# Kernel tuning notes

Hardware: AMD Instinct MI355X
Metric: run time of the kernel (lower is better)

The kernel has to match this reference:

```python
import jax, jax.numpy as jnp
import numpy as np

B, S, D, H = 4, 2048, 512, 8
HD = D // H  # head_dim = 64


def setup_inputs() -> dict:
    key = jax.random.key(0)
    ks = jax.random.split(key, 10)
    scale = 1.0 / np.sqrt(D)  # keep activations O(1)
    x = jax.random.normal(ks[0], (B, S, D), dtype=jnp.float32)
    # causal mask, broadcast over batch and heads
    causal = jnp.tril(jnp.ones((S, S), dtype=bool))
    mask = jnp.broadcast_to(causal, (B, H, S, S))
    def lin(k):
        return jax.random.normal(k, (D, D), dtype=jnp.float32) * scale
    return {
        "x": x,
        "mask": mask,
        "Wq": lin(ks[1]), "bq": jax.random.normal(ks[2], (D,), dtype=jnp.float32) * 0.01,
        "Wk": lin(ks[3]), "bk": jax.random.normal(ks[4], (D,), dtype=jnp.float32) * 0.01,
        "Wv": lin(ks[5]), "bv": jax.random.normal(ks[6], (D,), dtype=jnp.float32) * 0.01,
        "Wo": lin(ks[7]), "bo": jax.random.normal(ks[8], (D,), dtype=jnp.float32) * 0.01,
    }


def reference(x, mask, Wq, bq, Wk, bk, Wv, bv, Wo, bo):
    # eqx.nn.Linear computes W @ x + b per row; batched form is x @ W.T + b.
    b, s, d = x.shape
    q = jnp.einsum("bsd,ed->bse", x, Wq) + bq
    k = jnp.einsum("bsd,ed->bse", x, Wk) + bk
    v = jnp.einsum("bsd,ed->bse", x, Wv) + bv
    # [B, H, S, HD]
    q = q.reshape(b, s, H, HD).transpose(0, 2, 1, 3)
    k = k.reshape(b, s, H, HD).transpose(0, 2, 1, 3)
    v = v.reshape(b, s, H, HD).transpose(0, 2, 1, 3)
    scores = jnp.einsum("bhqd,bhkd->bhqk", q, k) / jnp.sqrt(jnp.asarray(HD, x.dtype))
    scores = jnp.where(mask, scores, jnp.asarray(-1e9, x.dtype))
    attn = jax.nn.softmax(scores, axis=-1)
    attended = jnp.einsum("bhqk,bhkd->bhqd", attn, v)
    attended = attended.transpose(0, 2, 1, 3).reshape(b, s, d)
    out = jnp.einsum("bsd,ed->bse", attended, Wo) + bo
    return out
```

## Files before the change

### kernel.cpp

```cpp
#include <hip/hip_runtime.h>

#define S_LEN 2048
#define DM    512
#define NH    8
#define HD    64

typedef unsigned short u16;
typedef unsigned int   u32;
typedef __bf16 bf16_t;
typedef bf16_t bf16x8 __attribute__((ext_vector_type(8)));
typedef float  f32x4  __attribute__((ext_vector_type(4)));

__device__ __forceinline__ u16 f2bf(float f) {
    u32 u = __float_as_uint(f);
    u += 0x7FFFu + ((u >> 16) & 1u);
    return (u16)(u >> 16);
}

__device__ __forceinline__ void g2l16(const u16* g, u16* l) {
    __builtin_amdgcn_global_load_lds(
        (const __attribute__((address_space(1))) u32*)g,
        (__attribute__((address_space(3))) u32*)l,
        16, 0, 0);
}

__device__ __forceinline__ float qmax16(float v) {
    v = fmaxf(v, __shfl_xor(v, 1));
    v = fmaxf(v, __shfl_xor(v, 2));
    v = fmaxf(v, __shfl_xor(v, 4));
    v = fmaxf(v, __shfl_xor(v, 8));
    return v;
}
__device__ __forceinline__ float qsum16(float v) {
    v += __shfl_xor(v, 1);
    v += __shfl_xor(v, 2);
    v += __shfl_xor(v, 4);
    v += __shfl_xor(v, 8);
    return v;
}

__global__ __launch_bounds__(256) void cvt_bf16(
    const float* __restrict__ x,
    const float* __restrict__ wq, const float* __restrict__ wk,
    const float* __restrict__ wv, const float* __restrict__ wo,
    u16* __restrict__ xb, u16* __restrict__ wqb, u16* __restrict__ wkb,
    u16* __restrict__ wvb, u16* __restrict__ wob)
{
    const int y = blockIdx.y;
    const float* src; u16* dst; int n;
    if (y == 0)      { src = x;  dst = xb;  n = 4 * S_LEN * DM; }
    else if (y == 1) { src = wq; dst = wqb; n = DM * DM; }
    else if (y == 2) { src = wk; dst = wkb; n = DM * DM; }
    else if (y == 3) { src = wv; dst = wvb; n = DM * DM; }
    else             { src = wo; dst = wob; n = DM * DM; }
    int idx = (blockIdx.x * 256 + threadIdx.x) * 8;
    if (idx >= n) return;
    float4 f0 = *(const float4*)(src + idx);
    float4 f1 = *(const float4*)(src + idx + 4);
    u32 p0 = (u32)f2bf(f0.x) | ((u32)f2bf(f0.y) << 16);
    u32 p1 = (u32)f2bf(f0.z) | ((u32)f2bf(f0.w) << 16);
    u32 p2 = (u32)f2bf(f1.x) | ((u32)f2bf(f1.y) << 16);
    u32 p3 = (u32)f2bf(f1.z) | ((u32)f2bf(f1.w) << 16);
    *(uint4*)(dst + idx) = make_uint4(p0, p1, p2, p3);
}

__global__ __launch_bounds__(256) void qkv_gemm(
    const u16* __restrict__ xb,
    const u16* __restrict__ Wqb, const u16* __restrict__ Wkb, const u16* __restrict__ Wvb,
    const float* __restrict__ bq, const float* __restrict__ bk, const float* __restrict__ bv,
    u16* __restrict__ Qb, u16* __restrict__ Kb, u16* __restrict__ Vb)
{
    __shared__ u16 Als[4096];
    __shared__ u16 Bls[4096];

    const int t = threadIdx.x;
    const int lane = t & 63, w = t >> 6;
    const int ln = lane & 15, quad = lane >> 4;
    const int wm = w >> 1, wn = w & 1;
    const int m0 = blockIdx.x * 128;
    const int mat = blockIdx.y >> 2;
    const int n0 = (blockIdx.y & 3) * 128;

    const u16* __restrict__ Wb     = (mat == 0) ? Wqb : (mat == 1) ? Wkb : Wvb;
    const float* __restrict__ bias = (mat == 0) ? bq : (mat == 1) ? bk : bv;
    u16* __restrict__ outp         = (mat == 0) ? Qb : (mat == 1) ? Kb : Vb;

    const int ch0 = (w * 2 + 0) * 64 + lane;
    const int ch1 = (w * 2 + 1) * 64 + lane;
    const int sr0 = ch0 >> 2, sk0 = (ch0 & 3) ^ ((sr0 >> 1) & 3);
    const int sr1 = ch1 >> 2, sk1 = (ch1 & 3) ^ ((sr1 >> 1) & 3);
    const u16* pA0 = xb + (size_t)(m0 + sr0) * DM + sk0 * 8;
    const u16* pA1 = xb + (size_t)(m0 + sr1) * DM + sk1 * 8;
    const u16* pB0 = Wb + (size_t)(n0 + sr0) * DM + sk0 * 8;
    const u16* pB1 = Wb + (size_t)(n0 + sr1) * DM + sk1 * 8;
    u16* lds0 = (u16*)((w * 2 + 0) * 512);
    u16* lds1 = (u16*)((w * 2 + 1) * 512);
    u16* lA0 = Als + (w * 2 + 0) * 512;
    u16* lA1 = Als + (w * 2 + 1) * 512;
    u16* lB0 = Bls + (w * 2 + 0) * 512;
    u16* lB1 = Bls + (w * 2 + 1) * 512;
    (void)lds0; (void)lds1;

    f32x4 acc[4][4] = {};
    for (int k0 = 0; k0 < DM; k0 += 32) {
        __syncthreads();
        g2l16(pA0 + k0, lA0);
        g2l16(pA1 + k0, lA1);
        g2l16(pB0 + k0, lB0);
        g2l16(pB1 + k0, lB1);
        __syncthreads();
        bf16x8 af[4], bf8[4];
        #pragma unroll
        for (int i = 0; i < 4; ++i) {
            int row = wm * 64 + i * 16 + ln;
            af[i] = *(const bf16x8*)(Als + (row * 4 + (quad ^ ((row >> 1) & 3))) * 8);
        }
        #pragma unroll
        for (int j = 0; j < 4; ++j) {
            int row = wn * 64 + j * 16 + ln;
            bf8[j] = *(const bf16x8*)(Bls + (row * 4 + (quad ^ ((row >> 1) & 3))) * 8);
        }
        #pragma unroll
        for (int i = 0; i < 4; ++i)
            #pragma unroll
            for (int j = 0; j < 4; ++j)
                acc[i][j] = __builtin_amdgcn_mfma_f32_16x16x32_bf16(af[i], bf8[j], acc[i][j], 0, 0, 0);
    }

    #pragma unroll
    for (int j = 0; j < 4; ++j) {
        int colg = n0 + wn * 64 + j * 16 + ln;
        float bj = bias[colg];
        int h = colg >> 6, d = colg & 63;
        #pragma unroll
        for (int i = 0; i < 4; ++i) {
            int mbase = m0 + wm * 64 + i * 16 + quad * 4;
            #pragma unroll
            for (int r = 0; r < 4; ++r) {
                int m = mbase + r;
                int bb = m >> 11, s = m & 2047;
                outp[(((size_t)bb * NH + h) * S_LEN + s) * HD + d] = f2bf(acc[i][j][r] + bj);
            }
        }
    }
}

__global__ __launch_bounds__(256) void attn_mfma(
    const u16* __restrict__ Qb, const u16* __restrict__ Kb, const u16* __restrict__ Vb,
    u16* __restrict__ Attb)
{
    __shared__ u16 Qls[4096];
    __shared__ u16 Kls[4096];
    __shared__ u16 Vt[4096];
    __shared__ u16 Ps[4096];

    const int t = threadIdx.x;
    const int lane = t & 63, w = t >> 6;
    const int ln = lane & 15, quad = lane >> 4;
    const int bh = blockIdx.y;
    const int qt = (blockIdx.x + bh) & 31;
    const int q_base = qt * 64;
    const size_t base = (size_t)bh * S_LEN * HD;

    {
        const int c0 = (w * 2 + 0) * 64 + lane;
        const int c1 = (w * 2 + 1) * 64 + lane;
        const int r0 = c0 >> 3, k0 = (c0 & 7) ^ (r0 & 7);
        const int r1 = c1 >> 3, k1 = (c1 & 7) ^ (r1 & 7);
        g2l16(Qb + base + (size_t)(q_base + r0) * HD + k0 * 8, Qls + (w * 2 + 0) * 512);
        g2l16(Qb + base + (size_t)(q_base + r1) * HD + k1 * 8, Qls + (w * 2 + 1) * 512);
    }
    __syncthreads();

    bf16x8 aq[2];
    #pragma unroll
    for (int ks = 0; ks < 2; ++ks) {
        int row = w * 16 + ln;
        aq[ks] = *(const bf16x8*)(Qls + (row * 8 + ((ks * 4 + quad) ^ (row & 7))) * 8);
    }

    const int ck0 = (w * 2 + 0) * 64 + lane;
    const int ck1 = (w * 2 + 1) * 64 + lane;
    const int kr0 = ck0 >> 3, kk0 = (ck0 & 7) ^ (kr0 & 7);
    const int kr1 = ck1 >> 3, kk1 = (ck1 & 7) ^ (kr1 & 7);
    const u16* pK0 = Kb + base + (size_t)kr0 * HD + kk0 * 8;
    const u16* pK1 = Kb + base + (size_t)kr1 * HD + kk1 * 8;
    u16* lK0 = Kls + (w * 2 + 0) * 512;
    u16* lK1 = Kls + (w * 2 + 1) * 512;

    const int vkey0 = t >> 3,        vd0 = (t & 7) * 8;
    const int vkey1 = (t + 256) >> 3;
    const u16* pV0 = Vb + base + (size_t)vkey0 * HD + vd0;
    const u16* pV1 = Vb + base + (size_t)vkey1 * HD + vd0;

    float m_st[4], l_st[4], alpha[4];
    f32x4 o[4] = {};
    #pragma unroll
    for (int r = 0; r < 4; ++r) { m_st[r] = -1e30f; l_st[r] = 0.f; }

    const float sc = 0.125f * 1.44269504f;
    const int qrow_base = q_base + w * 16;

    for (int kt = 0; kt <= qt; ++kt) {
        __syncthreads();
        g2l16(pK0 + (size_t)kt * 64 * HD, lK0);
        g2l16(pK1 + (size_t)kt * 64 * HD, lK1);
        {
            uint4 vv0 = *(const uint4*)(pV0 + (size_t)kt * 64 * HD);
            uint4 vv1 = *(const uint4*)(pV1 + (size_t)kt * 64 * HD);
            u16 ve[8];
            *(uint4*)ve = vv0;
            int kvq = vkey0 >> 3, kvl = vkey0 & 7;
            #pragma unroll
            for (int ii = 0; ii < 8; ++ii) {
                int i = (ii + (t & 7)) & 7;
                int d = vd0 + i;
                Vt[(d * 8 + (kvq ^ (d & 7))) * 8 + kvl] = ve[i];
            }
            *(uint4*)ve = vv1;
            kvq = vkey1 >> 3; kvl = vkey1 & 7;
            #pragma unroll
            for (int ii = 0; ii < 8; ++ii) {
                int i = (ii + (t & 7)) & 7;
                int d = vd0 + i;
                Vt[(d * 8 + (kvq ^ (d & 7))) * 8 + kvl] = ve[i];
            }
        }
        __syncthreads();

        f32x4 s[4] = {};
        #pragma unroll
        for (int ks = 0; ks < 2; ++ks)
            #pragma unroll
            for (int j = 0; j < 4; ++j) {
                int krow = j * 16 + ln;
                bf16x8 bk8 = *(const bf16x8*)(Kls + (krow * 8 + ((ks * 4 + quad) ^ (krow & 7))) * 8);
                s[j] = __builtin_amdgcn_mfma_f32_16x16x32_bf16(aq[ks], bk8, s[j], 0, 0, 0);
            }

        if (kt == qt) {
            #pragma unroll
            for (int j = 0; j < 4; ++j)
                #pragma unroll
                for (int r = 0; r < 4; ++r) {
                    int qg = qrow_base + quad * 4 + r;
                    int kg = kt * 64 + j * 16 + ln;
                    s[j][r] = (kg > qg) ? -1e30f : s[j][r] * sc;
                }
        } else {
            #pragma unroll
            for (int j = 0; j < 4; ++j)
                #pragma unroll
                for (int r = 0; r < 4; ++r)
                    s[j][r] *= sc;
        }

        #pragma unroll
        for (int r = 0; r < 4; ++r) {
            float mx = fmaxf(fmaxf(s[0][r], s[1][r]), fmaxf(s[2][r], s[3][r]));
            mx = qmax16(mx);
            float mnew = fmaxf(m_st[r], mx);
            float al = __builtin_amdgcn_exp2f(m_st[r] - mnew);
            m_st[r] = mnew;
            float rs = 0.f;
            #pragma unroll
            for (int j = 0; j < 4; ++j) {
                float p = __builtin_amdgcn_exp2f(s[j][r] - mnew);
                s[j][r] = p;
                rs += p;
            }
            rs = qsum16(rs);
            l_st[r] = l_st[r] * al + rs;
            alpha[r] = al;
        }
        #pragma unroll
        for (int j = 0; j < 4; ++j)
            #pragma unroll
            for (int r = 0; r < 4; ++r)
                o[j][r] *= alpha[r];

        #pragma unroll
        for (int j = 0; j < 4; ++j) {
            int key = j * 16 + ln;
            int kq = key >> 3, kl = key & 7;
            #pragma unroll
            for (int r = 0; r < 4; ++r) {
                int qrow = w * 16 + quad * 4 + r;
                Ps[(qrow * 8 + (kq ^ (qrow & 7))) * 8 + kl] = f2bf(s[j][r]);
            }
        }

        #pragma unroll
        for (int ks = 0; ks < 2; ++ks) {
            int kqg = ks * 4 + quad;
            int prow = w * 16 + ln;
            bf16x8 pa = *(const bf16x8*)(Ps + (prow * 8 + (kqg ^ (prow & 7))) * 8);
            #pragma unroll
            for (int j = 0; j < 4; ++j) {
                int rowd = j * 16 + ln;
                bf16x8 vb8 = *(const bf16x8*)(Vt + (rowd * 8 + (kqg ^ (rowd & 7))) * 8);
                o[j] = __builtin_amdgcn_mfma_f32_16x16x32_bf16(pa, vb8, o[j], 0, 0, 0);
            }
        }
    }

    const int bb = bh >> 3, h = bh & 7;
    #pragma unroll
    for (int r = 0; r < 4; ++r) {
        int qg = q_base + w * 16 + quad * 4 + r;
        float inv = 1.f / l_st[r];
        #pragma unroll
        for (int j = 0; j < 4; ++j) {
            int d = j * 16 + ln;
            Attb[((size_t)(bb * S_LEN + qg)) * DM + h * HD + d] = f2bf(o[j][r] * inv);
        }
    }
}

__global__ __launch_bounds__(256) void out_gemm(
    const u16* __restrict__ Ab, const u16* __restrict__ Wob,
    const float* __restrict__ bo, float* __restrict__ out)
{
    __shared__ u16 Als[4096];
    __shared__ u16 Bls[4096];

    const int t = threadIdx.x;
    const int lane = t & 63, w = t >> 6;
    const int ln = lane & 15, quad = lane >> 4;
    const int wm = w >> 1, wn = w & 1;
    const int m0 = blockIdx.x * 128;
    const int n0 = blockIdx.y * 128;

    const int ch0 = (w * 2 + 0) * 64 + lane;
    const int ch1 = (w * 2 + 1) * 64 + lane;
    const int sr0 = ch0 >> 2, sk0 = (ch0 & 3) ^ ((sr0 >> 1) & 3);
    const int sr1 = ch1 >> 2, sk1 = (ch1 & 3) ^ ((sr1 >> 1) & 3);
    const u16* pA0 = Ab  + (size_t)(m0 + sr0) * DM + sk0 * 8;
    const u16* pA1 = Ab  + (size_t)(m0 + sr1) * DM + sk1 * 8;
    const u16* pB0 = Wob + (size_t)(n0 + sr0) * DM + sk0 * 8;
    const u16* pB1 = Wob + (size_t)(n0 + sr1) * DM + sk1 * 8;
    u16* lA0 = Als + (w * 2 + 0) * 512;
    u16* lA1 = Als + (w * 2 + 1) * 512;
    u16* lB0 = Bls + (w * 2 + 0) * 512;
    u16* lB1 = Bls + (w * 2 + 1) * 512;

    f32x4 acc[4][4] = {};
    for (int k0 = 0; k0 < DM; k0 += 32) {
        __syncthreads();
        g2l16(pA0 + k0, lA0);
        g2l16(pA1 + k0, lA1);
        g2l16(pB0 + k0, lB0);
        g2l16(pB1 + k0, lB1);
        __syncthreads();
        bf16x8 af[4], bf8[4];
        #pragma unroll
        for (int i = 0; i < 4; ++i) {
            int row = wm * 64 + i * 16 + ln;
            af[i] = *(const bf16x8*)(Als + (row * 4 + (quad ^ ((row >> 1) & 3))) * 8);
        }
        #pragma unroll
        for (int j = 0; j < 4; ++j) {
            int row = wn * 64 + j * 16 + ln;
            bf8[j] = *(const bf16x8*)(Bls + (row * 4 + (quad ^ ((row >> 1) & 3))) * 8);
        }
        #pragma unroll
        for (int i = 0; i < 4; ++i)
            #pragma unroll
            for (int j = 0; j < 4; ++j)
                acc[i][j] = __builtin_amdgcn_mfma_f32_16x16x32_bf16(af[i], bf8[j], acc[i][j], 0, 0, 0);
    }

    #pragma unroll
    for (int j = 0; j < 4; ++j) {
        int colg = n0 + wn * 64 + j * 16 + ln;
        float bj = bo[colg];
        #pragma unroll
        for (int i = 0; i < 4; ++i) {
            int mbase = m0 + wm * 64 + i * 16 + quad * 4;
            #pragma unroll
            for (int r = 0; r < 4; ++r) {
                int m = mbase + r;
                out[(size_t)m * DM + colg] = acc[i][j][r] + bj;
            }
        }
    }
}

extern "C" void kernel_launch(void* const* d_in, const int* in_sizes, int n_in,
                              void* d_out, int out_size, void* d_ws, size_t ws_size,
                              hipStream_t stream) {
    const float* x  = (const float*)d_in[0];
    const float* Wq = (const float*)d_in[2];
    const float* bq = (const float*)d_in[3];
    const float* Wk = (const float*)d_in[4];
    const float* bk = (const float*)d_in[5];
    const float* Wv = (const float*)d_in[6];
    const float* bv = (const float*)d_in[7];
    const float* Wo = (const float*)d_in[8];
    const float* bo = (const float*)d_in[9];
    float* out = (float*)d_out;

    u16* ws = (u16*)d_ws;
    const size_t NX = (size_t)4 * S_LEN * DM;
    const size_t NW = (size_t)DM * DM;
    u16* xb   = ws;
    u16* wqb  = xb + NX;
    u16* wkb  = wqb + NW;
    u16* wvb  = wkb + NW;
    u16* wob  = wvb + NW;
    u16* Qb   = wob + NW;
    u16* Kb   = Qb + NX;
    u16* Vb   = Kb + NX;
    u16* Attb = Vb + NX;

    cvt_bf16<<<dim3(2048, 5), 256, 0, stream>>>(x, Wq, Wk, Wv, Wo, xb, wqb, wkb, wvb, wob);
    qkv_gemm<<<dim3(64, 12), 256, 0, stream>>>(xb, wqb, wkb, wvb, bq, bk, bv, Qb, Kb, Vb);
    attn_mfma<<<dim3(32, 32), 256, 0, stream>>>(Qb, Kb, Vb, Attb);
    out_gemm<<<dim3(64, 4), 256, 0, stream>>>(Attb, wob, bo, out);
}
```

Measured before the change: 776.4 us.

## Double-buffer LDS tiles in GEMM and attention kernels to overlap loads

Adds ping-pong LDS buffers to qkv_gemm, out_gemm and attn_mfma. The first tile is prefetched before the loop, and each iteration issues the next tile's global-to-LDS loads before computing on the current buffer. This drops one barrier per iteration and is meant to hide global memory latency behind the MFMA work. In the attention kernel the register-staged V transpose is now written into the next buffer after the QK^T MFMAs. The cost is double the LDS footprint for the K/V and GEMM tiles, which may lower occupancy. Correctness relies on the single remaining barrier also waiting for the async LDS loads to finish.

```diff
diff --git a/kernel.cpp b/kernel.cpp
--- a/kernel.cpp
+++ b/kernel.cpp
@@ -70,8 +70,8 @@
     const float* __restrict__ bq, const float* __restrict__ bk, const float* __restrict__ bv,
     u16* __restrict__ Qb, u16* __restrict__ Kb, u16* __restrict__ Vb)
 {
-    __shared__ u16 Als[4096];
-    __shared__ u16 Bls[4096];
+    __shared__ u16 Als[2][4096];
+    __shared__ u16 Bls[2][4096];
 
     const int t = threadIdx.x;
     const int lane = t & 63, w = t >> 6;
@@ -93,32 +93,35 @@
     const u16* pA1 = xb + (size_t)(m0 + sr1) * DM + sk1 * 8;
     const u16* pB0 = Wb + (size_t)(n0 + sr0) * DM + sk0 * 8;
     const u16* pB1 = Wb + (size_t)(n0 + sr1) * DM + sk1 * 8;
-    u16* lds0 = (u16*)((w * 2 + 0) * 512);
-    u16* lds1 = (u16*)((w * 2 + 1) * 512);
-    u16* lA0 = Als + (w * 2 + 0) * 512;
-    u16* lA1 = Als + (w * 2 + 1) * 512;
-    u16* lB0 = Bls + (w * 2 + 0) * 512;
-    u16* lB1 = Bls + (w * 2 + 1) * 512;
-    (void)lds0; (void)lds1;
+    const int lo0 = (w * 2 + 0) * 512;
+    const int lo1 = (w * 2 + 1) * 512;
+
+    g2l16(pA0, &Als[0][lo0]);
+    g2l16(pA1, &Als[0][lo1]);
+    g2l16(pB0, &Bls[0][lo0]);
+    g2l16(pB1, &Bls[0][lo1]);
 
     f32x4 acc[4][4] = {};
-    for (int k0 = 0; k0 < DM; k0 += 32) {
+    for (int it = 0; it < 16; ++it) {
+        const int cur = it & 1, nxt = cur ^ 1;
         __syncthreads();
-        g2l16(pA0 + k0, lA0);
-        g2l16(pA1 + k0, lA1);
-        g2l16(pB0 + k0, lB0);
-        g2l16(pB1 + k0, lB1);
-        __syncthreads();
+        if (it + 1 < 16) {
+            const int k0n = (it + 1) * 32;
+            g2l16(pA0 + k0n, &Als[nxt][lo0]);
+            g2l16(pA1 + k0n, &Als[nxt][lo1]);
+            g2l16(pB0 + k0n, &Bls[nxt][lo0]);
+            g2l16(pB1 + k0n, &Bls[nxt][lo1]);
+        }
         bf16x8 af[4], bf8[4];
         #pragma unroll
         for (int i = 0; i < 4; ++i) {
             int row = wm * 64 + i * 16 + ln;
-            af[i] = *(const bf16x8*)(Als + (row * 4 + (quad ^ ((row >> 1) & 3))) * 8);
+            af[i] = *(const bf16x8*)(&Als[cur][0] + (row * 4 + (quad ^ ((row >> 1) & 3))) * 8);
         }
         #pragma unroll
         for (int j = 0; j < 4; ++j) {
             int row = wn * 64 + j * 16 + ln;
-            bf8[j] = *(const bf16x8*)(Bls + (row * 4 + (quad ^ ((row >> 1) & 3))) * 8);
+            bf8[j] = *(const bf16x8*)(&Bls[cur][0] + (row * 4 + (quad ^ ((row >> 1) & 3))) * 8);
         }
         #pragma unroll
         for (int i = 0; i < 4; ++i)
@@ -150,8 +153,8 @@
     u16* __restrict__ Attb)
 {
     __shared__ u16 Qls[4096];
-    __shared__ u16 Kls[4096];
-    __shared__ u16 Vt[4096];
+    __shared__ u16 Kls[2][4096];
+    __shared__ u16 Vt[2][4096];
     __shared__ u16 Ps[4096];
 
     const int t = threadIdx.x;
@@ -162,13 +165,46 @@
     const int q_base = qt * 64;
     const size_t base = (size_t)bh * S_LEN * HD;
 
+    const int c0 = (w * 2 + 0) * 64 + lane;
+    const int c1 = (w * 2 + 1) * 64 + lane;
+    const int r0 = c0 >> 3, k0s = (c0 & 7) ^ (r0 & 7);
+    const int r1 = c1 >> 3, k1s = (c1 & 7) ^ (r1 & 7);
+    const int lo0 = (w * 2 + 0) * 512;
+    const int lo1 = (w * 2 + 1) * 512;
+
+    g2l16(Qb + base + (size_t)(q_base + r0) * HD + k0s * 8, Qls + lo0);
+    g2l16(Qb + base + (size_t)(q_base + r1) * HD + k1s * 8, Qls + lo1);
+
+    const u16* pK0 = Kb + base + (size_t)r0 * HD + k0s * 8;
+    const u16* pK1 = Kb + base + (size_t)r1 * HD + k1s * 8;
+    g2l16(pK0, &Kls[0][lo0]);
+    g2l16(pK1, &Kls[0][lo1]);
+
+    const int vkey0 = t >> 3, vd0 = (t & 7) * 8;
+    const int vkey1 = (t + 256) >> 3;
+    const u16* pV0 = Vb + base + (size_t)vkey0 * HD + vd0;
+    const u16* pV1 = Vb + base + (size_t)vkey1 * HD + vd0;
+    const int kvq0 = vkey0 >> 3, kvl0 = vkey0 & 7;
+    const int kvq1 = vkey1 >> 3, kvl1 = vkey1 & 7;
+
     {
-        const int c0 = (w * 2 + 0) * 64 + lane;
-        const int c1 = (w * 2 + 1) * 64 + lane;
-        const int r0 = c0 >> 3, k0 = (c0 & 7) ^ (r0 & 7);
-        const int r1 = c1 >> 3, k1 = (c1 & 7) ^ (r1 & 7);
-        g2l16(Qb + base + (size_t)(q_base + r0) * HD + k0 * 8, Qls + (w * 2 + 0) * 512);
-        g2l16(Qb + base + (size_t)(q_base + r1) * HD + k1 * 8, Qls + (w * 2 + 1) * 512);
+        uint4 vv0 = *(const uint4*)(pV0);
+        uint4 vv1 = *(const uint4*)(pV1);
+        u16 ve[8];
+        *(uint4*)ve = vv0;
+        #pragma unroll
+        for (int ii = 0; ii < 8; ++ii) {
+            int i = (ii + (t & 7)) & 7;
+            int d = vd0 + i;
+            Vt[0][(d * 8 + (kvq0 ^ (d & 7))) * 8 + kvl0] = ve[i];
+        }
+        *(uint4*)ve = vv1;
+        #pragma unroll
+        for (int ii = 0; ii < 8; ++ii) {
+            int i = (ii + (t & 7)) & 7;
+            int d = vd0 + i;
+            Vt[0][(d * 8 + (kvq1 ^ (d & 7))) * 8 + kvl1] = ve[i];
+        }
     }
     __syncthreads();
 
@@ -179,20 +215,6 @@
         aq[ks] = *(const bf16x8*)(Qls + (row * 8 + ((ks * 4 + quad) ^ (row & 7))) * 8);
     }
 
-    const int ck0 = (w * 2 + 0) * 64 + lane;
-    const int ck1 = (w * 2 + 1) * 64 + lane;
-    const int kr0 = ck0 >> 3, kk0 = (ck0 & 7) ^ (kr0 & 7);
-    const int kr1 = ck1 >> 3, kk1 = (ck1 & 7) ^ (kr1 & 7);
-    const u16* pK0 = Kb + base + (size_t)kr0 * HD + kk0 * 8;
-    const u16* pK1 = Kb + base + (size_t)kr1 * HD + kk1 * 8;
-    u16* lK0 = Kls + (w * 2 + 0) * 512;
-    u16* lK1 = Kls + (w * 2 + 1) * 512;
-
-    const int vkey0 = t >> 3,        vd0 = (t & 7) * 8;
-    const int vkey1 = (t + 256) >> 3;
-    const u16* pV0 = Vb + base + (size_t)vkey0 * HD + vd0;
-    const u16* pV1 = Vb + base + (size_t)vkey1 * HD + vd0;
-
     float m_st[4], l_st[4], alpha[4];
     f32x4 o[4] = {};
     #pragma unroll
@@ -202,41 +224,46 @@
     const int qrow_base = q_base + w * 16;
 
     for (int kt = 0; kt <= qt; ++kt) {
+        const int cur = kt & 1, nxt = cur ^ 1;
         __syncthreads();
-        g2l16(pK0 + (size_t)kt * 64 * HD, lK0);
-        g2l16(pK1 + (size_t)kt * 64 * HD, lK1);
-        {
-            uint4 vv0 = *(const uint4*)(pV0 + (size_t)kt * 64 * HD);
-            uint4 vv1 = *(const uint4*)(pV1 + (size_t)kt * 64 * HD);
+
+        uint4 vv0, vv1;
+        const bool more = (kt < qt);
+        if (more) {
+            const size_t off = (size_t)(kt + 1) * 64 * HD;
+            g2l16(pK0 + off, &Kls[nxt][lo0]);
+            g2l16(pK1 + off, &Kls[nxt][lo1]);
+            vv0 = *(const uint4*)(pV0 + off);
+            vv1 = *(const uint4*)(pV1 + off);
+        }
+
+        f32x4 s[4] = {};
+        #pragma unroll
+        for (int ks = 0; ks < 2; ++ks)
+            #pragma unroll
+            for (int j = 0; j < 4; ++j) {
+                int krow = j * 16 + ln;
+                bf16x8 bk8 = *(const bf16x8*)(&Kls[cur][0] + (krow * 8 + ((ks * 4 + quad) ^ (krow & 7))) * 8);
+                s[j] = __builtin_amdgcn_mfma_f32_16x16x32_bf16(aq[ks], bk8, s[j], 0, 0, 0);
+            }
+
+        if (more) {
             u16 ve[8];
             *(uint4*)ve = vv0;
-            int kvq = vkey0 >> 3, kvl = vkey0 & 7;
             #pragma unroll
             for (int ii = 0; ii < 8; ++ii) {
                 int i = (ii + (t & 7)) & 7;
                 int d = vd0 + i;
-                Vt[(d * 8 + (kvq ^ (d & 7))) * 8 + kvl] = ve[i];
+                Vt[nxt][(d * 8 + (kvq0 ^ (d & 7))) * 8 + kvl0] = ve[i];
             }
             *(uint4*)ve = vv1;
-            kvq = vkey1 >> 3; kvl = vkey1 & 7;
             #pragma unroll
             for (int ii = 0; ii < 8; ++ii) {
                 int i = (ii + (t & 7)) & 7;
                 int d = vd0 + i;
-                Vt[(d * 8 + (kvq ^ (d & 7))) * 8 + kvl] = ve[i];
-            }
-        }
-        __syncthreads();
-
-        f32x4 s[4] = {};
-        #pragma unroll
-        for (int ks = 0; ks < 2; ++ks)
-            #pragma unroll
-            for (int j = 0; j < 4; ++j) {
-                int krow = j * 16 + ln;
-                bf16x8 bk8 = *(const bf16x8*)(Kls + (krow * 8 + ((ks * 4 + quad) ^ (krow & 7))) * 8);
-                s[j] = __builtin_amdgcn_mfma_f32_16x16x32_bf16(aq[ks], bk8, s[j], 0, 0, 0);
-            }
+                Vt[nxt][(d * 8 + (kvq1 ^ (d & 7))) * 8 + kvl1] = ve[i];
+            }
+        }
 
         if (kt == qt) {
             #pragma unroll
@@ -298,7 +325,7 @@
             #pragma unroll
             for (int j = 0; j < 4; ++j) {
                 int rowd = j * 16 + ln;
-                bf16x8 vb8 = *(const bf16x8*)(Vt + (rowd * 8 + (kqg ^ (rowd & 7))) * 8);
+                bf16x8 vb8 = *(const bf16x8*)(&Vt[cur][0] + (rowd * 8 + (kqg ^ (rowd & 7))) * 8);
                 o[j] = __builtin_amdgcn_mfma_f32_16x16x32_bf16(pa, vb8, o[j], 0, 0, 0);
             }
         }
@@ -321,8 +348,8 @@
     const u16* __restrict__ Ab, const u16* __restrict__ Wob,
     const float* __restrict__ bo, float* __restrict__ out)
 {
-    __shared__ u16 Als[4096];
-    __shared__ u16 Bls[4096];
+    __shared__ u16 Als[2][4096];
+    __shared__ u16 Bls[2][4096];
 
     const int t = threadIdx.x;
     const int lane = t & 63, w = t >> 6;
@@ -339,29 +366,35 @@
     const u16* pA1 = Ab  + (size_t)(m0 + sr1) * DM + sk1 * 8;
     const u16* pB0 = Wob + (size_t)(n0 + sr0) * DM + sk0 * 8;
     const u16* pB1 = Wob + (size_t)(n0 + sr1) * DM + sk1 * 8;
-    u16* lA0 = Als + (w * 2 + 0) * 512;
-    u16* lA1 = Als + (w * 2 + 1) * 512;
-    u16* lB0 = Bls + (w * 2 + 0) * 512;
-    u16* lB1 = Bls + (w * 2 + 1) * 512;
+    const int lo0 = (w * 2 + 0) * 512;
+    const int lo1 = (w * 2 + 1) * 512;
+
+    g2l16(pA0, &Als[0][lo0]);
+    g2l16(pA1, &Als[0][lo1]);
+    g2l16(pB0, &Bls[0][lo0]);
+    g2l16(pB1, &Bls[0][lo1]);
 
     f32x4 acc[4][4] = {};
-    for (int k0 = 0; k0 < DM; k0 += 32) {
+    for (int it = 0; it < 16; ++it) {
+        const int cur = it & 1, nxt = cur ^ 1;
         __syncthreads();
-        g2l16(pA0 + k0, lA0);
-        g2l16(pA1 + k0, lA1);
-        g2l16(pB0 + k0, lB0);
-        g2l16(pB1 + k0, lB1);
-        __syncthreads();
+        if (it + 1 < 16) {
+            const int k0n = (it + 1) * 32;
+            g2l16(pA0 + k0n, &Als[nxt][lo0]);
+            g2l16(pA1 + k0n, &Als[nxt][lo1]);
+            g2l16(pB0 + k0n, &Bls[nxt][lo0]);
+            g2l16(pB1 + k0n, &Bls[nxt][lo1]);
+        }
         bf16x8 af[4], bf8[4];
         #pragma unroll
         for (int i = 0; i < 4; ++i) {
             int row = wm * 64 + i * 16 + ln;
-            af[i] = *(const bf16x8*)(Als + (row * 4 + (quad ^ ((row >> 1) & 3))) * 8);
+            af[i] = *(const bf16x8*)(&Als[cur][0] + (row * 4 + (quad ^ ((row >> 1) & 3))) * 8);
         }
         #pragma unroll
         for (int j = 0; j < 4; ++j) {
             int row = wn * 64 + j * 16 + ln;
-            bf8[j] = *(const bf16x8*)(Bls + (row * 4 + (quad ^ ((row >> 1) & 3))) * 8);
+            bf8[j] = *(const bf16x8*)(&Bls[cur][0] + (row * 4 + (quad ^ ((row >> 1) & 3))) * 8);
         }
         #pragma unroll
         for (int i = 0; i < 4; ++i)
```

New measurement: 749.4 us. 1.04x faster.
